# Optimization experiments

Hardware: AMD Instinct MI355X
Metric: run time of the kernel (lower is better)

The kernel has to match this reference:

```python
import jax, jax.numpy as jnp
import numpy as np

H = 64  # lstm hidden size
SLOPE = 0.01  # LeakyReLU default negative slope


def _leaky(x):
    return jnp.where(x >= 0, x, SLOPE * x)


def setup_inputs() -> dict:
    key = jax.random.key(0)
    ks = jax.random.split(key, 20)
    B, T = 32768, 200
    s = 0.1
    inp = {
        "noise": jax.random.normal(ks[0], (B, 3), jnp.float32),
        "w_ih0": jax.random.normal(ks[1], (4 * H, 3), jnp.float32) * s,
        "w_hh0": jax.random.normal(ks[2], (4 * H, H), jnp.float32) * s,
        "b_ih0": jax.random.normal(ks[3], (4 * H,), jnp.float32) * s,
        "b_hh0": jax.random.normal(ks[4], (4 * H,), jnp.float32) * s,
        "w_ih1": jax.random.normal(ks[5], (4 * H, H), jnp.float32) * s,
        "w_hh1": jax.random.normal(ks[6], (4 * H, H), jnp.float32) * s,
        "b_ih1": jax.random.normal(ks[7], (4 * H,), jnp.float32) * s,
        "b_hh1": jax.random.normal(ks[8], (4 * H,), jnp.float32) * s,
        "w_ih2": jax.random.normal(ks[9], (4 * H, H), jnp.float32) * s,
        "w_hh2": jax.random.normal(ks[10], (4 * H, H), jnp.float32) * s,
        "b_ih2": jax.random.normal(ks[11], (4 * H,), jnp.float32) * s,
        "b_hh2": jax.random.normal(ks[12], (4 * H,), jnp.float32) * s,
        "w1": jax.random.normal(ks[13], (32, H), jnp.float32) * s,
        "b1": jax.random.normal(ks[14], (32,), jnp.float32) * s,
        "w2": jax.random.normal(ks[15], (16, 32), jnp.float32) * s,
        "b2": jax.random.normal(ks[16], (16,), jnp.float32) * s,
        "w3": jax.random.normal(ks[17], (3, 16), jnp.float32) * s,
        "b3": jax.random.normal(ks[18], (3,), jnp.float32) * s,
        "length": T,
    }
    return inp


def _forward(noise, w_ih0, w_hh0, b_ih0, b_hh0, w_ih1, w_hh1, b_ih1, b_hh1,
             w_ih2, w_hh2, b_ih2, b_hh2, w1, b1, w2, b2, w3, b3, length):
    B = noise.shape[0]
    layers = [(w_ih0, w_hh0, b_ih0, b_hh0),
              (w_ih1, w_hh1, b_ih1, b_hh1),
              (w_ih2, w_hh2, b_ih2, b_hh2)]

    def cell(x, h, c, wih, whh, bih, bhh):
        # PyTorch LSTM gate order: i, f, g, o
        g = x @ wih.T + h @ whh.T + (bih + bhh)
        i, f, gg, o = jnp.split(g, 4, axis=-1)
        c_new = jax.nn.sigmoid(f) * c + jax.nn.sigmoid(i) * jnp.tanh(gg)
        h_new = jax.nn.sigmoid(o) * jnp.tanh(c_new)
        return h_new, c_new

    def step(carry, _):
        x, hs, cs = carry  # x: (B,3), hs/cs: (3,B,H)
        inp = x
        new_h, new_c = [], []
        for l, (wih, whh, bih, bhh) in enumerate(layers):
            h, c = cell(inp, hs[l], cs[l], wih, whh, bih, bhh)
            new_h.append(h)
            new_c.append(c)
            inp = h
        # MLP head (Dropout is identity in eval; LeakyReLU slope 0.01)
        y = _leaky(inp @ w1.T + b1)
        y = _leaky(y @ w2.T + b2)
        y = _leaky(y @ w3.T + b3)  # (B, 3)
        return (y, jnp.stack(new_h), jnp.stack(new_c)), y

    hs0 = jnp.zeros((3, B, H), noise.dtype)
    cs0 = jnp.zeros((3, B, H), noise.dtype)
    (_, _, _), ys = jax.lax.scan(step, (noise, hs0, cs0), None, length=length)
    return jnp.transpose(ys, (1, 0, 2))  # (B, T, 3)


def reference(noise, w_ih0, w_hh0, b_ih0, b_hh0, w_ih1, w_hh1, b_ih1, b_hh1,
              w_ih2, w_hh2, b_ih2, b_hh2, w1, b1, w2, b2, w3, b3, length):
    return _forward(noise, w_ih0, w_hh0, b_ih0, b_hh0, w_ih1, w_hh1, b_ih1,
                    b_hh1, w_ih2, w_hh2, b_ih2, b_hh2, w1, b1, w2, b2, w3,
                    b3, length)
```

## Files before the change

kernel.cpp:

```cpp
#include <hip/hip_runtime.h>

typedef __attribute__((ext_vector_type(4))) float  f32x4;
typedef __attribute__((ext_vector_type(8))) short  bf16x8;
typedef __attribute__((ext_vector_type(4))) short  bf16x4;

#define NTHR 1024
#define BT   128
#define L2E  1.4426950408889634f

#define PLANE(L)   ((L)*16384)
#define QS(s)      (49152 + (s)*16384)
#define XFB_OFF    131072
#define Y1_OFF     133120
#define Y2_OFF     142336
#define BGL_OFF    146944
#define W0L_OFF    150016
#define B3L_OFF    154112
#define W3L_OFF    154128
#define W1L_OFF    154320
#define W2L_OFF    158416
#define OUT_OFF    159440
#define LDS_TOTAL  162512

__device__ __align__(16) unsigned char g_wsbuf[163840];

__device__ __forceinline__ unsigned short f2bf(float v) {
    unsigned int x = __float_as_uint(v);
    unsigned int r = x + 0x7fffu + ((x >> 16) & 1u);
    return (unsigned short)(r >> 16);
}
__device__ __forceinline__ float bf2f_lo(unsigned int d) { return __uint_as_float(d << 16); }
__device__ __forceinline__ float bf2f_hi(unsigned int d) { return __uint_as_float(d & 0xffff0000u); }

__device__ __forceinline__ float fsig2(float y) {
    return __builtin_amdgcn_rcpf(1.0f + __builtin_amdgcn_exp2f(-y));
}
__device__ __forceinline__ float ftanh2(float y) {
    return 1.0f - 2.0f * __builtin_amdgcn_rcpf(1.0f + __builtin_amdgcn_exp2f(y));
}
__device__ __forceinline__ float ftanhc(float c) {
    return 1.0f - 2.0f * __builtin_amdgcn_rcpf(1.0f + __builtin_amdgcn_exp2f(c * (2.0f * L2E)));
}

__global__ void prep_weights(const float* __restrict__ whh0, const float* __restrict__ wih1,
                             const float* __restrict__ whh1, const float* __restrict__ wih2,
                             const float* __restrict__ whh2)
{
    int gi = blockIdx.x * 256 + threadIdx.x;
    if (gi < 10240) {
        int m = gi / 2048;
        int rem = gi & 2047;
        int b = rem >> 6, l = rem & 63;
        int ks = b & 1, g = (b >> 1) & 3, ug = b >> 3;
        int row = g * 64 + ug * 16 + (l & 15);
        int kb  = ks * 32 + (l >> 4) * 8;
        float fac = (g == 2) ? (2.0f * L2E) : L2E;
        const float* src = (m == 0) ? whh0 : (m == 1) ? wih1 : (m == 2) ? whh1
                         : (m == 3) ? wih2 : whh2;
        unsigned short o[8];
        #pragma unroll
        for (int i = 0; i < 8; ++i)
            o[i] = f2bf(src[row * 64 + kb + i] * fac);
        unsigned char* dst = g_wsbuf + m * 32768 + b * 1024 + l * 16;
        #pragma unroll
        for (int i = 0; i < 8; ++i) ((unsigned short*)dst)[i] = o[i];
    }
}

#define MFMA_(A,B,C) __builtin_amdgcn_mfma_f32_16x16x32_bf16(A, B, C, 0, 0, 0)

#define BARX do { \
    asm volatile("s_waitcnt lgkmcnt(0)" ::: "memory"); \
    __builtin_amdgcn_s_barrier(); \
    __builtin_amdgcn_sched_barrier(0); \
    } while (0)

#define LOADQ(m, ks, R) \
    R = *(const bf16x8*)(g_wsbuf + (m) * 32768 + \
        ((tid >> 6) * 2 + (ks)) * 1024 + (tid & 63) * 16)
#define COMMITQ(R, BUF) \
    *(bf16x8*)(lds + (BUF) + tid * 16) = R

#define ACC_INIT(L, ACC) do { \
    _Pragma("unroll") for (int g_ = 0; g_ < 4; ++g_) { \
        float b_ = *(const float*)(lds + BGL_OFF + ((L) * 256 + g_ * 64 + u) * 4); \
        f32x4 t_ = {b_, b_, b_, b_}; \
        ACC[g_][0] = t_; ACC[g_][1] = t_; \
    } } while (0)

#define GATEP(ACC, APL, ks, BUF) do { \
    bf16x8 b_[4]; \
    _Pragma("unroll") for (int g_ = 0; g_ < 4; ++g_) \
        b_[g_] = *(const bf16x8*)(lds + (BUF) + (ug * 4 + g_) * 1024 + lane * 16); \
    _Pragma("unroll") for (int mt_ = 0; mt_ < 2; ++mt_) { \
        int ab_ = (((mbase + mt_ * 16 + l15) * 128 + (ks) * 64 + l4 * 16)) ^ rswz; \
        bf16x8 ah_ = *(const bf16x8*)(lds + PLANE(APL) + ab_); \
        _Pragma("unroll") for (int g_ = 0; g_ < 4; ++g_) \
            ACC[g_][mt_] = MFMA_(ah_, b_[g_], ACC[g_][mt_]); \
    } } while (0)

#define CELLW(L, CARR, ACC) do { \
    _Pragma("unroll") for (int mt_ = 0; mt_ < 2; ++mt_) \
    _Pragma("unroll") for (int r_ = 0; r_ < 4; ++r_) { \
        float gi_ = fsig2(ACC[0][mt_][r_]); \
        float gf_ = fsig2(ACC[1][mt_][r_]); \
        float gg_ = ftanh2(ACC[2][mt_][r_]); \
        float go_ = fsig2(ACC[3][mt_][r_]); \
        float cn_ = gf_ * CARR[mt_ * 4 + r_] + gi_ * gg_; \
        CARR[mt_ * 4 + r_] = cn_; \
        float hn_ = go_ * ftanhc(cn_); \
        int e_ = mbase + mt_ * 16 + l4 * 4 + r_; \
        int wb_ = ((e_ * 128 + u * 2)) ^ ((e_ & 7) << 4); \
        *(unsigned short*)(lds + PLANE(L) + wb_) = f2bf(hn_); \
    } } while (0)

#define XPART(ACC) do { \
    _Pragma("unroll") for (int mt_ = 0; mt_ < 2; ++mt_) \
    _Pragma("unroll") for (int r_ = 0; r_ < 4; ++r_) { \
        int e_ = mbase + mt_ * 16 + l4 * 4 + r_; \
        f32x4 xv_ = *(const f32x4*)(lds + XFB_OFF + e_ * 16); \
        _Pragma("unroll") for (int g_ = 0; g_ < 4; ++g_) { \
            f32x4 w0_ = *(const f32x4*)(lds + W0L_OFF + (g_ * 64 + u) * 16); \
            ACC[g_][mt_][r_] += xv_.x * w0_.x + xv_.y * w0_.y + xv_.z * w0_.z; \
        } } } while (0)

#define MLP1 do { \
    int Mt_ = wv >> 1; \
    f32x4 a1_ = {b1r, b1r, b1r, b1r}; \
    bf16x8 wh0_ = *(const bf16x8*)(lds + W1L_OFF + (hf * 2 + 0) * 1024 + lane * 16); \
    bf16x8 wh1_ = *(const bf16x8*)(lds + W1L_OFF + (hf * 2 + 1) * 1024 + lane * 16); \
    { int ab_ = (((Mt_ * 16 + l15) * 128 + 0 * 64 + l4 * 16)) ^ rswz; \
      bf16x8 ah_ = *(const bf16x8*)(lds + PLANE(2) + ab_); \
      a1_ = MFMA_(ah_, wh0_, a1_); } \
    { int ab_ = (((Mt_ * 16 + l15) * 128 + 1 * 64 + l4 * 16)) ^ rswz; \
      bf16x8 ah_ = *(const bf16x8*)(lds + PLANE(2) + ab_); \
      a1_ = MFMA_(ah_, wh1_, a1_); } \
    _Pragma("unroll") for (int r_ = 0; r_ < 4; ++r_) { \
        float y_ = a1_[r_]; y_ = (y_ >= 0.f) ? y_ : 0.01f * y_; \
        int e_ = Mt_ * 16 + l4 * 4 + r_; \
        *(unsigned short*)(lds + Y1_OFF + e_ * 72 + hf * 32 + l15 * 2) = f2bf(y_); \
    } } while (0)

#define MLP2M do { \
    if (wv < 8) { \
        bf16x4 alo_ = *(const bf16x4*)(lds + Y1_OFF + (wv * 16 + l15) * 72 + l4 * 16); \
        bf16x4 ahi_ = *(const bf16x4*)(lds + Y1_OFF + (wv * 16 + l15) * 72 + l4 * 16 + 8); \
        bf16x8 af_ = {alo_[0], alo_[1], alo_[2], alo_[3], \
                      ahi_[0], ahi_[1], ahi_[2], ahi_[3]}; \
        bf16x8 w2f_ = *(const bf16x8*)(lds + W2L_OFF + (l15 * 32 + l4 * 8) * 2); \
        f32x4 a2_ = {b2r, b2r, b2r, b2r}; \
        a2_ = MFMA_(af_, w2f_, a2_); \
        _Pragma("unroll") for (int r_ = 0; r_ < 4; ++r_) { \
            float y_ = a2_[r_]; y_ = (y_ >= 0.f) ? y_ : 0.01f * y_; \
            int e_ = wv * 16 + l4 * 4 + r_; \
            *(unsigned short*)(lds + Y2_OFF + e_ * 36 + l15 * 2) = f2bf(y_); \
        } } } while (0)

#define MLP3_OUT(tc) do { \
    if (tid < 384) { \
        int e3_ = tid & 127, r3_ = tid >> 7; \
        float a3_ = *(const float*)(lds + B3L_OFF + r3_ * 4); \
        _Pragma("unroll") for (int kd_ = 0; kd_ < 8; ++kd_) { \
            unsigned int d_ = *(const unsigned int*)(lds + Y2_OFF + e3_ * 36 + kd_ * 4); \
            a3_ = fmaf(bf2f_lo(d_), *(const float*)(lds + W3L_OFF + (r3_ * 16 + kd_ * 2) * 4),     a3_); \
            a3_ = fmaf(bf2f_hi(d_), *(const float*)(lds + W3L_OFF + (r3_ * 16 + kd_ * 2 + 1) * 4), a3_); \
        } \
        float y_ = (a3_ >= 0.f) ? a3_ : 0.01f * a3_; \
        *(float*)(lds + XFB_OFF + e3_ * 16 + r3_ * 4) = y_; \
        *(float*)(lds + OUT_OFF + e3_ * 24 + ((tc) & 1) * 12 + r3_ * 4) = y_; \
    } } while (0)

extern "C" __global__ void __launch_bounds__(NTHR)
__attribute__((amdgpu_waves_per_eu(4, 4)))
lstm_mfma(const float* __restrict__ noise,
          const float* __restrict__ wih0, const float* __restrict__ whh0,
          const float* __restrict__ bih0, const float* __restrict__ bhh0,
          const float* __restrict__ wih1, const float* __restrict__ whh1,
          const float* __restrict__ bih1, const float* __restrict__ bhh1,
          const float* __restrict__ wih2, const float* __restrict__ whh2,
          const float* __restrict__ bih2, const float* __restrict__ bhh2,
          const float* __restrict__ w1g, const float* __restrict__ b1g,
          const float* __restrict__ w2g, const float* __restrict__ b2g,
          const float* __restrict__ w3g, const float* __restrict__ b3g,
          const int* __restrict__ lenp, float* __restrict__ out)
{
    extern __shared__ unsigned char lds[];
    const int tid  = threadIdx.x;
    const int lane = tid & 63;
    const int wv   = tid >> 6;
    const int ug   = wv & 3;
    const int mh   = wv >> 2;
    const int l15  = lane & 15;
    const int l4   = lane >> 4;
    const int u    = ug * 16 + l15;
    const int mbase = mh * 32;
    const int rswz  = (lane & 7) << 4;
    const int hf    = wv & 1;
    const int T = *lenp;
    const long eg0  = (long)blockIdx.x * BT;
    const long outs = 3L * T;

    float c0[8], c1[8], c2[8];
    #pragma unroll
    for (int i = 0; i < 8; ++i) { c0[i] = 0.f; c1[i] = 0.f; c2[i] = 0.f; }

    const float b1r = b1g[hf * 16 + l15];
    const float b2r = b2g[l15];

    bf16x8 Ra, Rb;

    LOADQ(2, 0, Ra);
    LOADQ(2, 1, Rb);

    for (int i = tid; i < 49152 / 4; i += NTHR) ((unsigned int*)lds)[i] = 0u;
    if (tid < BT) {
        const float* np = noise + (eg0 + tid) * 3;
        f32x4 xv = {np[0], np[1], np[2], 0.f};
        *(f32x4*)(lds + XFB_OFF + tid * 16) = xv;
    }
    if (tid < 768) {
        int l = tid >> 8, r = tid & 255, g = r >> 6;
        float fac = (g == 2) ? (2.0f * L2E) : L2E;
        const float* bi = (l == 0) ? bih0 : ((l == 1) ? bih1 : bih2);
        const float* bh = (l == 0) ? bhh0 : ((l == 1) ? bhh1 : bhh2);
        *(float*)(lds + BGL_OFF + tid * 4) = (bi[r] + bh[r]) * fac;
    }
    if (tid < 256) {
        int g = tid >> 6;
        float fac = (g == 2) ? (2.0f * L2E) : L2E;
        f32x4 wv0 = {wih0[tid * 3] * fac, wih0[tid * 3 + 1] * fac,
                     wih0[tid * 3 + 2] * fac, 0.f};
        *(f32x4*)(lds + W0L_OFF + tid * 16) = wv0;
    }
    if (tid < 256) {
        int b = tid >> 6, l = tid & 63;
        int hh = b >> 1, ks = b & 1;
        int row = hh * 16 + (l & 15);
        int kb  = ks * 32 + (l >> 4) * 8;
        unsigned short o[8];
        #pragma unroll
        for (int i = 0; i < 8; ++i) o[i] = f2bf(w1g[row * 64 + kb + i]);
        #pragma unroll
        for (int i = 0; i < 8; ++i)
            *(unsigned short*)(lds + W1L_OFF + b * 1024 + l * 16 + i * 2) = o[i];
    }
    if (tid < 512) *(unsigned short*)(lds + W2L_OFF + tid * 2) = f2bf(w2g[tid]);
    if (tid < 3)   *(float*)(lds + B3L_OFF + tid * 4) = b3g[tid];
    if (tid < 48)  *(float*)(lds + W3L_OFF + tid * 4) = w3g[tid];

    __syncthreads();
    COMMITQ(Ra, QS(0));
    COMMITQ(Rb, QS(1));
    LOADQ(1, 0, Ra);
    LOADQ(1, 1, Rb);
    COMMITQ(Ra, QS(2));
    COMMITQ(Rb, QS(3));
    LOADQ(4, 0, Ra);

    f32x4 accA[4][2], accB[4][2];
    ACC_INIT(0, accA);
    __syncthreads();

    #pragma unroll 1
    for (int t = 0; t < T; ++t) {
        COMMITQ(Ra, QS(4)); LOADQ(4, 1, Ra);
        XPART(accA); CELLW(0, c0, accA);
        ACC_INIT(1, accB); GATEP(accB, 1, 0, QS(0));
        BARX;
        COMMITQ(Ra, QS(0)); LOADQ(3, 0, Ra);
        GATEP(accB, 1, 1, QS(1)); GATEP(accB, 0, 0, QS(2));
        BARX;
        COMMITQ(Ra, QS(1)); LOADQ(3, 1, Ra); LOADQ(0, 1, Rb);
        GATEP(accB, 0, 1, QS(3));
        ACC_INIT(2, accA); GATEP(accA, 2, 0, QS(4));
        BARX;
        COMMITQ(Ra, QS(2)); COMMITQ(Rb, QS(4)); LOADQ(0, 0, Ra);
        CELLW(1, c1, accB);
        GATEP(accA, 2, 1, QS(0));
        BARX;
        COMMITQ(Ra, QS(3)); LOADQ(2, 0, Ra);
        GATEP(accA, 1, 0, QS(1)); GATEP(accA, 1, 1, QS(2));
        BARX;
        COMMITQ(Ra, QS(0)); LOADQ(2, 1, Ra);
        CELLW(2, c2, accA);
        ACC_INIT(0, accB); GATEP(accB, 0, 0, QS(3));
        BARX;
        COMMITQ(Ra, QS(1)); LOADQ(1, 0, Ra);
        MLP1;
        GATEP(accB, 0, 1, QS(4));
        BARX;
        COMMITQ(Ra, QS(2)); LOADQ(1, 1, Ra);
        MLP2M;
        BARX;
        COMMITQ(Ra, QS(3)); LOADQ(4, 0, Ra);
        MLP3_OUT(t);
        if ((t & 1) == 1) {
            BARX;
            long tb = t - 1;
            if (tid < 768) {
                int e = tid / 6, rem = tid - e * 6;
                int st = rem / 3, j = rem - st * 3;
                out[(eg0 + e) * outs + (tb + st) * 3 + j] =
                    *(const float*)(lds + OUT_OFF + e * 24 + st * 12 + j * 4);
            }
        }
        BARX;
        #pragma unroll
        for (int g = 0; g < 4; ++g) {
            accA[g][0] = accB[g][0];
            accA[g][1] = accB[g][1];
        }
    }

    if (T & 1) {
        if (tid < 384) {
            int e = tid & 127, j = tid >> 7;
            out[(eg0 + e) * outs + (long)(T - 1) * 3 + j] =
                *(const float*)(lds + OUT_OFF + e * 24 + ((T - 1) & 1) * 12 + j * 4);
        }
    }
}

extern "C" void kernel_launch(void* const* d_in, const int* in_sizes, int n_in,
                              void* d_out, int out_size, void* d_ws, size_t ws_size,
                              hipStream_t stream)
{
    const float* noise = (const float*)d_in[0];
    const float* wih0  = (const float*)d_in[1];
    const float* whh0  = (const float*)d_in[2];
    const float* bih0  = (const float*)d_in[3];
    const float* bhh0  = (const float*)d_in[4];
    const float* wih1  = (const float*)d_in[5];
    const float* whh1  = (const float*)d_in[6];
    const float* bih1  = (const float*)d_in[7];
    const float* bhh1  = (const float*)d_in[8];
    const float* wih2  = (const float*)d_in[9];
    const float* whh2  = (const float*)d_in[10];
    const float* bih2  = (const float*)d_in[11];
    const float* bhh2  = (const float*)d_in[12];
    const float* w1g   = (const float*)d_in[13];
    const float* b1g   = (const float*)d_in[14];
    const float* w2g   = (const float*)d_in[15];
    const float* b2g   = (const float*)d_in[16];
    const float* w3g   = (const float*)d_in[17];
    const float* b3g   = (const float*)d_in[18];
    const int*   lenp  = (const int*)d_in[19];
    float* out = (float*)d_out;

    int B = in_sizes[0] / 3;
    int grid = B / BT;

    prep_weights<<<40, 256, 0, stream>>>(whh0, wih1, whh1, wih2, whh2);

    hipFuncSetAttribute((const void*)lstm_mfma,
                        hipFuncAttributeMaxDynamicSharedMemorySize, LDS_TOTAL);
    lstm_mfma<<<grid, NTHR, LDS_TOTAL, stream>>>(
        noise, wih0, whh0, bih0, bhh0, wih1, whh1, bih1, bhh1,
        wih2, whh2, bih2, bhh2, w1g, b1g, w2g, b2g, w3g, b3g, lenp, out);
}
```

Before: 4.230 ms.

## Reschedule LSTM step to single accumulator set and restructure weight streaming

```diff
diff --git a/kernel.cpp b/kernel.cpp
--- a/kernel.cpp
+++ b/kernel.cpp
@@ -81,14 +81,14 @@
 #define COMMITQ(R, BUF) \
     *(bf16x8*)(lds + (BUF) + tid * 16) = R
 
-#define ACC_INIT(L, ACC) do { \
+#define ACC_INIT(L) do { \
     _Pragma("unroll") for (int g_ = 0; g_ < 4; ++g_) { \
         float b_ = *(const float*)(lds + BGL_OFF + ((L) * 256 + g_ * 64 + u) * 4); \
         f32x4 t_ = {b_, b_, b_, b_}; \
-        ACC[g_][0] = t_; ACC[g_][1] = t_; \
-    } } while (0)
-
-#define GATEP(ACC, APL, ks, BUF) do { \
+        acc[g_][0] = t_; acc[g_][1] = t_; \
+    } } while (0)
+
+#define GATEP(APL, ks, BUF) do { \
     bf16x8 b_[4]; \
     _Pragma("unroll") for (int g_ = 0; g_ < 4; ++g_) \
         b_[g_] = *(const bf16x8*)(lds + (BUF) + (ug * 4 + g_) * 1024 + lane * 16); \
@@ -96,16 +96,16 @@
         int ab_ = (((mbase + mt_ * 16 + l15) * 128 + (ks) * 64 + l4 * 16)) ^ rswz; \
         bf16x8 ah_ = *(const bf16x8*)(lds + PLANE(APL) + ab_); \
         _Pragma("unroll") for (int g_ = 0; g_ < 4; ++g_) \
-            ACC[g_][mt_] = MFMA_(ah_, b_[g_], ACC[g_][mt_]); \
-    } } while (0)
-
-#define CELLW(L, CARR, ACC) do { \
+            acc[g_][mt_] = MFMA_(ah_, b_[g_], acc[g_][mt_]); \
+    } } while (0)
+
+#define CELLW(L, CARR) do { \
     _Pragma("unroll") for (int mt_ = 0; mt_ < 2; ++mt_) \
     _Pragma("unroll") for (int r_ = 0; r_ < 4; ++r_) { \
-        float gi_ = fsig2(ACC[0][mt_][r_]); \
-        float gf_ = fsig2(ACC[1][mt_][r_]); \
-        float gg_ = ftanh2(ACC[2][mt_][r_]); \
-        float go_ = fsig2(ACC[3][mt_][r_]); \
+        float gi_ = fsig2(acc[0][mt_][r_]); \
+        float gf_ = fsig2(acc[1][mt_][r_]); \
+        float gg_ = ftanh2(acc[2][mt_][r_]); \
+        float go_ = fsig2(acc[3][mt_][r_]); \
         float cn_ = gf_ * CARR[mt_ * 4 + r_] + gi_ * gg_; \
         CARR[mt_ * 4 + r_] = cn_; \
         float hn_ = go_ * ftanhc(cn_); \
@@ -114,14 +114,14 @@
         *(unsigned short*)(lds + PLANE(L) + wb_) = f2bf(hn_); \
     } } while (0)
 
-#define XPART(ACC) do { \
+#define XPART do { \
     _Pragma("unroll") for (int mt_ = 0; mt_ < 2; ++mt_) \
     _Pragma("unroll") for (int r_ = 0; r_ < 4; ++r_) { \
         int e_ = mbase + mt_ * 16 + l4 * 4 + r_; \
         f32x4 xv_ = *(const f32x4*)(lds + XFB_OFF + e_ * 16); \
         _Pragma("unroll") for (int g_ = 0; g_ < 4; ++g_) { \
             f32x4 w0_ = *(const f32x4*)(lds + W0L_OFF + (g_ * 64 + u) * 16); \
-            ACC[g_][mt_][r_] += xv_.x * w0_.x + xv_.y * w0_.y + xv_.z * w0_.z; \
+            acc[g_][mt_][r_] += xv_.x * w0_.x + xv_.y * w0_.y + xv_.z * w0_.z; \
         } } } while (0)
 
 #define MLP1 do { \
@@ -252,47 +252,46 @@
     COMMITQ(Ra, QS(0));
     COMMITQ(Rb, QS(1));
     LOADQ(1, 0, Ra);
-    LOADQ(1, 1, Rb);
     COMMITQ(Ra, QS(2));
-    COMMITQ(Rb, QS(3));
-    LOADQ(4, 0, Ra);
-
-    f32x4 accA[4][2], accB[4][2];
-    ACC_INIT(0, accA);
+    LOADQ(1, 1, Ra);
+    LOADQ(4, 0, Rb);
+
+    f32x4 acc[4][2];
+    ACC_INIT(0);
     __syncthreads();
 
     #pragma unroll 1
     for (int t = 0; t < T; ++t) {
-        COMMITQ(Ra, QS(4)); LOADQ(4, 1, Ra);
-        XPART(accA); CELLW(0, c0, accA);
-        ACC_INIT(1, accB); GATEP(accB, 1, 0, QS(0));
-        BARX;
-        COMMITQ(Ra, QS(0)); LOADQ(3, 0, Ra);
-        GATEP(accB, 1, 1, QS(1)); GATEP(accB, 0, 0, QS(2));
-        BARX;
-        COMMITQ(Ra, QS(1)); LOADQ(3, 1, Ra); LOADQ(0, 1, Rb);
-        GATEP(accB, 0, 1, QS(3));
-        ACC_INIT(2, accA); GATEP(accA, 2, 0, QS(4));
-        BARX;
-        COMMITQ(Ra, QS(2)); COMMITQ(Rb, QS(4)); LOADQ(0, 0, Ra);
-        CELLW(1, c1, accB);
-        GATEP(accA, 2, 1, QS(0));
-        BARX;
-        COMMITQ(Ra, QS(3)); LOADQ(2, 0, Ra);
-        GATEP(accA, 1, 0, QS(1)); GATEP(accA, 1, 1, QS(2));
-        BARX;
-        COMMITQ(Ra, QS(0)); LOADQ(2, 1, Ra);
-        CELLW(2, c2, accA);
-        ACC_INIT(0, accB); GATEP(accB, 0, 0, QS(3));
-        BARX;
-        COMMITQ(Ra, QS(1)); LOADQ(1, 0, Ra);
+        COMMITQ(Ra, QS(3)); COMMITQ(Rb, QS(4));
+        LOADQ(4, 1, Ra); LOADQ(3, 0, Rb);
+        XPART; CELLW(0, c0);
+        ACC_INIT(1); GATEP(1, 0, QS(0));
+        BARX;
+        COMMITQ(Ra, QS(0)); LOADQ(3, 1, Ra);
+        GATEP(1, 1, QS(1)); GATEP(0, 0, QS(2));
+        BARX;
+        COMMITQ(Rb, QS(1)); COMMITQ(Ra, QS(2));
+        LOADQ(0, 0, Rb); LOADQ(0, 1, Ra);
+        GATEP(0, 1, QS(3));
+        CELLW(1, c1);
+        ACC_INIT(2); GATEP(2, 0, QS(4));
+        BARX;
+        COMMITQ(Rb, QS(3)); COMMITQ(Ra, QS(4));
+        LOADQ(2, 0, Rb); LOADQ(2, 1, Ra);
+        GATEP(2, 1, QS(0)); GATEP(1, 0, QS(1));
+        BARX;
+        COMMITQ(Rb, QS(0)); LOADQ(1, 0, Rb);
+        GATEP(1, 1, QS(2));
+        CELLW(2, c2);
+        ACC_INIT(0); GATEP(0, 0, QS(3));
+        BARX;
+        COMMITQ(Ra, QS(1)); LOADQ(1, 1, Ra);
+        GATEP(0, 1, QS(4));
         MLP1;
-        GATEP(accB, 0, 1, QS(4));
-        BARX;
-        COMMITQ(Ra, QS(2)); LOADQ(1, 1, Ra);
+        BARX;
+        COMMITQ(Rb, QS(2)); LOADQ(4, 0, Rb);
         MLP2M;
         BARX;
-        COMMITQ(Ra, QS(3)); LOADQ(4, 0, Ra);
         MLP3_OUT(t);
         if ((t & 1) == 1) {
             BARX;
@@ -305,11 +304,6 @@
             }
         }
         BARX;
-        #pragma unroll
-        for (int g = 0; g < 4; ++g) {
-            accA[g][0] = accB[g][0];
-            accA[g][1] = accB[g][1];
-        }
     }
 
     if (T & 1) {
```

Result: faster. 3.506 ms, median of 2 (-17.1%).
